# Optimization experiments

Hardware: AMD Instinct MI355X
Metric: run time of the kernel (lower is better)

Reference implementation:

```python
import jax, jax.numpy as jnp
import numpy as np
from jax.scipy.special import erf

F = 64          # scalar feature channels (hidden_irreps multiplicity)
S = 9           # spherical harmonics dim for max_ell=2
NB = 8          # num_bessel
RMAX = 5.0
PPOLY = 5       # num_polynomial_cutoff
AVG_NEIGH = 16.0
SIGMA = 1.0     # atomic_multipoles_smearing_width
KE = 1.0        # Coulomb constant (model units)
N = 20000; G = 20; E = 320000; NEL = 10; L = 2; HMLP = 16

def _sph_l2(u):
    # real spherical harmonics up to l=2, e3nn 'component' normalization,
    # with permute_to_e3nn_convention (y, z, x) ordering for l=1
    x, y, z = u[..., 0], u[..., 1], u[..., 2]
    s3 = 1.7320508075688772; s5 = 2.23606797749979; s15 = 3.872983346207417
    return jnp.stack([jnp.ones_like(x),
                      s3 * y, s3 * z, s3 * x,
                      s15 * x * y, s15 * y * z, 0.5 * s5 * (3.0 * z * z - 1.0),
                      s15 * x * z, 0.5 * s15 * (x * x - y * y)], axis=-1)

def _radial(r):
    # Bessel basis with smooth polynomial cutoff (p = PPOLY)
    n = jnp.arange(1, NB + 1, dtype=r.dtype)
    rb = jnp.sqrt(2.0 / RMAX) * jnp.sin(n * jnp.pi * r[:, None] / RMAX) / r[:, None]
    x = r / RMAX
    p = float(PPOLY)
    u = (1.0 - 0.5 * (p + 1.0) * (p + 2.0) * x**PPOLY
         + p * (p + 2.0) * x**(PPOLY + 1) - 0.5 * p * (p + 1.0) * x**(PPOLY + 2))
    u = jnp.where(x < 1.0, u, 0.0)
    return rb * u[:, None]

def setup_inputs() -> dict:
    key = jax.random.key(0)
    ks = jax.random.split(key, 20)
    Ng = N // G
    species = jax.random.randint(ks[0], (N,), 0, NEL)
    node_attrs = jax.nn.one_hot(species, NEL, dtype=jnp.float32)
    positions = jax.random.uniform(ks[1], (N, 3), dtype=jnp.float32) * 10.0
    g = jax.random.randint(ks[2], (E,), 0, G)
    s_loc = jax.random.randint(ks[3], (E,), 0, Ng)
    off = jax.random.randint(ks[4], (E,), 1, Ng)   # avoid self edges
    r_loc = (s_loc + off) % Ng
    edge_index = jnp.stack([g * Ng + s_loc, g * Ng + r_loc], axis=0)
    batch = jnp.repeat(jnp.arange(G), Ng)
    sc = 0.1
    atomic_energies = jax.random.normal(ks[5], (NEL,)) * sc
    embed_w = jax.random.normal(ks[6], (NEL, F)) * sc
    radial_w1 = jax.random.normal(ks[7], (L, NB, 64)) * 0.3
    radial_b1 = jnp.zeros((L, 64), jnp.float32)
    radial_w2 = jax.random.normal(ks[8], (L, 64, F)) * 0.2
    prod_w = jax.random.normal(ks[9], (L, NEL, F)) * 0.3
    readout_w = jax.random.normal(ks[10], (L, F)) * sc
    ro2_w1 = jax.random.normal(ks[11], (F, HMLP)) * 0.2
    ro2_b1 = jnp.zeros((HMLP,), jnp.float32)
    ro2_w2 = jax.random.normal(ks[12], (HMLP, 1)) * 0.2
    charge_w = jax.random.normal(ks[13], (L, F)) * sc
    flux_w = jax.random.normal(ks[14], (L, NB)) * sc
    formal_charges = jax.random.normal(ks[15], (NEL,)) * 0.5
    return dict(node_attrs=node_attrs, positions=positions, edge_index=edge_index,
                batch=batch, num_graphs=G, atomic_energies=atomic_energies,
                embed_w=embed_w, radial_w1=radial_w1, radial_b1=radial_b1,
                radial_w2=radial_w2, prod_w=prod_w, readout_w=readout_w,
                ro2_w1=ro2_w1, ro2_b1=ro2_b1, ro2_w2=ro2_w2,
                charge_w=charge_w, flux_w=flux_w, formal_charges=formal_charges)

def reference(node_attrs, positions, edge_index, batch, num_graphs,
              atomic_energies, embed_w, radial_w1, radial_b1, radial_w2,
              prod_w, readout_w, ro2_w1, ro2_b1, ro2_w2,
              charge_w, flux_w, formal_charges):
    Nn = node_attrs.shape[0]
    Ng = Nn // num_graphs
    snd, rcv = edge_index[0], edge_index[1]
    # atomic reference energies (E0) and node embedding
    node_e0 = node_attrs @ atomic_energies                      # [N]
    e0 = jax.ops.segment_sum(node_e0, batch, num_graphs)        # [G]
    node_scalars = node_attrs @ embed_w                         # [N,F]
    # edge geometry: gather, spherical harmonics, radial embedding
    vec = positions[rcv] - positions[snd]                       # [E,3]
    lengths = jnp.sqrt((vec * vec).sum(-1) + 1e-12)             # [E]
    unit = vec / lengths[:, None]
    edge_attrs = _sph_l2(unit)                                  # [E,S]
    edge_feats = _radial(lengths)                               # [E,NB]
    # formal charges (per-species)
    FQ = node_attrs @ formal_charges                            # [N]
    charge_density = FQ
    flux = jnp.zeros_like(lengths)
    energies = [e0]
    node_e_list = [node_e0]
    nL = radial_w1.shape[0]
    for l in range(nL):
        # interaction: radial MLP -> per-edge TP messages -> scatter sum
        R = jax.nn.silu(edge_feats @ radial_w1[l] + radial_b1[l]) @ radial_w2[l]  # [E,F]
        m = (R * node_scalars[snd])[:, :, None] * edge_attrs[:, None, :]          # [E,F,S]
        agg = jax.ops.segment_sum(m, rcv, Nn) / AVG_NEIGH                         # [N,F,S]
        # equivariant product (correlation-2 flavor) + element-dependent skip
        sk = node_scalars * (node_attrs @ prod_w[l])                              # [N,F]
        feats = agg + agg * agg[:, :, :1]                                         # [N,F,S]
        node_scalars = feats[:, :, 0] + sk                                        # [N,F]
        if l == nL - 1:
            node_energies = (jax.nn.silu(node_scalars @ ro2_w1 + ro2_b1) @ ro2_w2)[:, 0]
        else:
            node_energies = node_scalars @ readout_w[l]
        energies.append(jax.ops.segment_sum(node_energies, batch, num_graphs))
        node_e_list.append(node_energies)
        # long-range source maps: per-node charge + per-edge flux contributions
        charge_density = charge_density + node_scalars @ charge_w[l]
        flux = flux + edge_feats @ flux_w[l]
    contributions = jnp.stack(energies, -1)                     # [G, L+1]
    total_energy = contributions.sum(-1)                        # [G]
    node_energy = jnp.stack(node_e_list, -1).sum(-1)            # [N]
    # polarization: edge-flux dipole + formal-charge dipole
    pol = jax.ops.segment_sum(flux[:, None] * vec, batch[rcv], num_graphs)
    pol = pol + jax.ops.segment_sum(FQ[:, None] * positions, batch, num_graphs)
    # direct (non-PBC) screened Coulomb energy per graph, equal-size graphs
    q = charge_density.reshape(num_graphs, Ng)
    p = positions.reshape(num_graphs, Ng, 3)
    d = p[:, :, None, :] - p[:, None, :, :]
    r = jnp.sqrt((d * d).sum(-1) + 1e-12)
    kern = erf(r / (2.0 * SIGMA)) / r * (1.0 - jnp.eye(Ng, dtype=r.dtype))
    e_el = 0.5 * KE * jnp.einsum('gi,gij,gj->g', q, kern, q)
    total_energy = total_energy + e_el
    total_charge = jax.ops.segment_sum(charge_density, batch, num_graphs)
    return total_energy, node_energy, contributions, pol, total_charge
```

## Files before the change

kernel.cpp:

```cpp
#include <hip/hip_runtime.h>
#include <math.h>

#define NEL 10
#define FD 64
#define NBES 8
#define GG 20
#define HML 16
#define EGB 512
#define NUB 5000

typedef __attribute__((ext_vector_type(8))) short short8;
typedef __attribute__((ext_vector_type(4))) float f32x4;

__device__ __forceinline__ float wred(float v) {
    #pragma unroll
    for (int off = 32; off > 0; off >>= 1) v += __shfl_down(v, off, 64);
    return v;
}

__device__ __forceinline__ float silu(float h) {
    return h / (1.f + __expf(-h));
}

__device__ __forceinline__ unsigned short f2bf(float x) {
    unsigned int b = __float_as_uint(x);
    unsigned int r = (b + 0x7FFFu + ((b >> 16) & 1u)) >> 16;
    return (unsigned short)r;
}

__device__ __forceinline__ int xcd_swizzle(int bid, int nb) {
    int q = nb >> 3, r = nb & 7;
    int x = bid & 7, i = bid >> 3;
    return (x < r ? x * (q + 1) : r * (q + 1) + (x - r) * q) + i;
}

__global__ __launch_bounds__(256) void setup_k(
    const float* __restrict__ attrs, const float* __restrict__ ae,
    const float* __restrict__ fc, const float* __restrict__ embed_w,
    const int* __restrict__ eidx, int* __restrict__ spec,
    float* __restrict__ q, float* __restrict__ out,
    float* __restrict__ scal, float* __restrict__ agg0,
    int* __restrict__ cnt, int N_, int E_)
{
    int idx = blockIdx.x * 256 + threadIdx.x;
    int lane = threadIdx.x & 63;
    int n = idx >> 6;
    bool pred = (lane < NEL) && (attrs[(size_t)n * NEL + lane] > 0.5f);
    unsigned long long m = __ballot(pred);
    int sp = (int)__builtin_ctzll(m);
    scal[idx] = embed_w[sp * FD + lane];
    agg0[idx] = 0.f;
    if (lane == 0) { spec[n] = sp; q[n] = fc[sp]; out[GG + n] = ae[sp]; }
    if (idx < E_) atomicAdd(&cnt[eidx[E_ + idx]], 1);
    if (idx < GG) out[idx] = 0.f;
}

__global__ __launch_bounds__(1024) void scan_k(
    const int* __restrict__ cnt, int* __restrict__ cur,
    const float* __restrict__ w1, const float* __restrict__ w2,
    unsigned short* __restrict__ w1bf, unsigned short* __restrict__ w2bf, int N_)
{
    int t = threadIdx.x;
    #pragma unroll
    for (int ii = 0; ii < 8; ++ii) {
        int idx = ii * 1024 + t;
        int l = idx >> 12, rem = idx & 4095;
        int f = rem >> 6, k = rem & 63;
        w2bf[idx] = f2bf(w2[l * 4096 + k * 64 + f]);
    }
    {
        int l = t >> 9, rem = t & 511;
        int m = rem >> 3, j = rem & 7;
        w1bf[t] = f2bf(w1[l * 512 + j * 64 + m]);
    }
    __shared__ int wtot[16];
    int lane = t & 63, wid = t >> 6;
    int base = t * 20;
    int c[20]; int s = 0;
    bool full = (base + 20 <= N_);
    if (full) {
        #pragma unroll
        for (int i = 0; i < 5; ++i) {
            int4 v4 = *(const int4*)&cnt[base + i * 4];
            c[i*4+0] = v4.x; c[i*4+1] = v4.y; c[i*4+2] = v4.z; c[i*4+3] = v4.w;
        }
        #pragma unroll
        for (int i = 0; i < 20; ++i) s += c[i];
    } else {
        #pragma unroll
        for (int i = 0; i < 20; ++i) { int idx = base + i; c[i] = (idx < N_) ? cnt[idx] : 0; s += c[i]; }
    }
    int v = s;
    #pragma unroll
    for (int off = 1; off < 64; off <<= 1) {
        int u = __shfl_up(v, off, 64);
        if (lane >= off) v += u;
    }
    if (lane == 63) wtot[wid] = v;
    __syncthreads();
    if (wid == 0 && lane < 16) {
        int wv = wtot[lane];
        #pragma unroll
        for (int off = 1; off < 16; off <<= 1) {
            int u = __shfl_up(wv, off, 64);
            if (lane >= off) wv += u;
        }
        wtot[lane] = wv;
    }
    __syncthreads();
    int ex = (wid > 0 ? wtot[wid - 1] : 0) + (v - s);
    if (full) {
        int o[20];
        #pragma unroll
        for (int i = 0; i < 20; ++i) { o[i] = ex; ex += c[i]; }
        #pragma unroll
        for (int i = 0; i < 5; ++i)
            *(int4*)&cur[base + i * 4] = make_int4(o[i*4+0], o[i*4+1], o[i*4+2], o[i*4+3]);
    } else {
        #pragma unroll
        for (int i = 0; i < 20; ++i) {
            int idx = base + i;
            if (idx < N_) { cur[idx] = ex; ex += c[i]; }
        }
    }
}

__global__ __launch_bounds__(256) void geom_scatter_k(
    const float* __restrict__ pos, const int* __restrict__ eidx,
    const float* __restrict__ flux_w, int* __restrict__ cur,
    unsigned int* __restrict__ esd, float* __restrict__ polpart,
    int E_, int ng)
{
    __shared__ float lpol[GG * 3];
    int tid = threadIdx.x;
    for (int i = tid; i < GG * 3; i += 256) lpol[i] = 0.f;
    __syncthreads();
    float fw[NBES];
    #pragma unroll
    for (int i = 0; i < NBES; ++i) fw[i] = flux_w[i] + flux_w[NBES + i];
    const float PI = 3.14159265358979323846f;
    for (int e = blockIdx.x * 256 + tid; e < E_; e += EGB * 256) {
        int s = eidx[e], r = eidx[E_ + e];
        float dx = pos[(size_t)r*3+0] - pos[(size_t)s*3+0];
        float dy = pos[(size_t)r*3+1] - pos[(size_t)s*3+1];
        float dz = pos[(size_t)r*3+2] - pos[(size_t)s*3+2];
        float len = sqrtf(dx*dx + dy*dy + dz*dz + 1e-12f);
        float x = len * 0.2f;
        float u = 0.f;
        if (x < 1.f) {
            float x2 = x * x;
            float x5 = x2 * x2 * x;
            u = 1.f - 21.f * x5 + 35.f * x5 * x - 15.f * x5 * x2;
        }
        float pref = 0.6324555320336759f / len * u;
        float theta = PI * x;
        float s1, c1;
        __sincosf(theta, &s1, &c1);
        float c2 = 2.f * c1;
        float sp_ = 0.f, sn = s1;
        float flux = 0.f;
        unsigned int pk[4];
        #pragma unroll
        for (int i = 0; i < 4; ++i) {
            float r0 = pref * sn;
            float n1 = c2 * sn - sp_; sp_ = sn; sn = n1;
            float r1 = pref * sn;
            n1 = c2 * sn - sp_; sp_ = sn; sn = n1;
            flux += r0 * fw[2*i] + r1 * fw[2*i+1];
            pk[i] = (unsigned int)f2bf(r0) | ((unsigned int)f2bf(r1) << 16);
        }
        int p = atomicAdd(&cur[r], 1);
        size_t off = (size_t)p * 8;
        *(uint4*)&esd[off]     = make_uint4(pk[0], pk[1], pk[2], pk[3]);
        *(uint2*)&esd[off + 4] = make_uint2((unsigned int)s, (unsigned int)r);
        int g = r / ng;
        atomicAdd(&lpol[g*3+0], flux * dx);
        atomicAdd(&lpol[g*3+1], flux * dy);
        atomicAdd(&lpol[g*3+2], flux * dz);
    }
    __syncthreads();
    for (int i = tid; i < GG * 3; i += 256) polpart[blockIdx.x * (GG * 3) + i] = lpol[i];
}

__global__ __launch_bounds__(256, 6) void edge_mlp_k(
    const unsigned int* __restrict__ esd,
    const unsigned short* __restrict__ w1bf, const float* __restrict__ b1,
    const unsigned short* __restrict__ w2bf, const float* __restrict__ scal,
    float* __restrict__ agg0, int layer, int E_)
{
    __shared__ __align__(16) char smem[4][4352];
    int t = threadIdx.x, w = t >> 6, lane = t & 63;
    int mrow = lane & 15, quad = lane >> 4;
    int xb = xcd_swizzle(blockIdx.x, gridDim.x);
    int ebase = (xb * 4 + w) * 16;
    unsigned short* hw = (unsigned short*)smem[w];
    float* cw = (float*)smem[w];

    int2 sr = *(const int2*)&esd[(size_t)(ebase + mrow) * 8 + 4];
    int sv = sr.x, rv = sr.y;

    const short8 z8 = {0,0,0,0,0,0,0,0};
    short8 b_ef = z8;
    if (quad == 0) b_ef = *(const short8*)&esd[(size_t)(ebase + mrow) * 8];
    else if (quad == 1) b_ef[0] = (short)0x3F80;
    short8 a1f[4];
    #pragma unroll
    for (int nt = 0; nt < 4; ++nt) {
        a1f[nt] = z8;
        if (quad == 0) a1f[nt] = *(const short8*)&w1bf[layer * 512 + (nt * 16 + mrow) * 8];
        else if (quad == 1) a1f[nt][0] = (short)f2bf(b1[layer * FD + nt * 16 + mrow]);
    }

    f32x4 zf = {0.f, 0.f, 0.f, 0.f};
    #pragma unroll
    for (int nt = 0; nt < 4; ++nt) {
        f32x4 c1 = __builtin_amdgcn_mfma_f32_16x16x32_bf16(a1f[nt], b_ef, zf, 0, 0, 0);
        unsigned int p01 = (unsigned int)f2bf(silu(c1[0])) | ((unsigned int)f2bf(silu(c1[1])) << 16);
        unsigned int p23 = (unsigned int)f2bf(silu(c1[2])) | ((unsigned int)f2bf(silu(c1[3])) << 16);
        *(uint2*)&hw[mrow * 72 + nt * 16 + quad * 4] = make_uint2(p01, p23);
    }

    const unsigned short* wb = w2bf + layer * 4096;
    short8 bf0[4], bf1[4];
    #pragma unroll
    for (int nt = 0; nt < 4; ++nt) {
        bf0[nt] = *(const short8*)&wb[(nt * 16 + mrow) * 64 + quad * 8];
        bf1[nt] = *(const short8*)&wb[(nt * 16 + mrow) * 64 + 32 + quad * 8];
    }

    short8 a0  = *(const short8*)&hw[mrow * 72 + quad * 8];
    short8 a1b = *(const short8*)&hw[mrow * 72 + 32 + quad * 8];
    f32x4 c[4];
    #pragma unroll
    for (int nt = 0; nt < 4; ++nt) {
        f32x4 cc = __builtin_amdgcn_mfma_f32_16x16x32_bf16(a0, bf0[nt], zf, 0, 0, 0);
        cc = __builtin_amdgcn_mfma_f32_16x16x32_bf16(a1b, bf1[nt], cc, 0, 0, 0);
        c[nt] = cc;
    }
    #pragma unroll
    for (int nt = 0; nt < 4; ++nt)
        #pragma unroll
        for (int reg = 0; reg < 4; ++reg)
            cw[(quad * 4 + reg) * 68 + nt * 16 + mrow] = c[nt][reg];

    int curR = __builtin_amdgcn_readlane(rv, 0);
    float run = 0.f;
    #pragma unroll
    for (int half = 0; half < 2; ++half) {
        float cv[8], sw[8];
        #pragma unroll
        for (int k = 0; k < 8; ++k) {
            int pp = half * 8 + k;
            cv[k] = cw[pp * 68 + lane];
            int s = __builtin_amdgcn_readlane(sv, pp);
            sw[k] = scal[(size_t)s * FD + lane];
        }
        #pragma unroll
        for (int k = 0; k < 8; ++k) {
            int pp = half * 8 + k;
            int r = __builtin_amdgcn_readlane(rv, pp);
            float v = cv[k] * sw[k];
            if (r != curR) {
                atomicAdd(&agg0[(size_t)curR * FD + lane], run);
                run = v; curR = r;
            } else {
                run += v;
            }
        }
    }
    atomicAdd(&agg0[(size_t)curR * FD + lane], run);
}

__global__ __launch_bounds__(256) void node_update_k(
    float* __restrict__ scal, float* __restrict__ agg0,
    const int* __restrict__ spec, const float* __restrict__ prod_w,
    const float* __restrict__ readout_w, const float* __restrict__ ro2_w1,
    const float* __restrict__ ro2_b1, const float* __restrict__ ro2_w2,
    const float* __restrict__ charge_w, float* __restrict__ q,
    float* __restrict__ out_nodeE, float* __restrict__ nEpart,
    int layer, int last, int N_)
{
    __shared__ float vsh[4][FD];
    __shared__ float red[4];
    int wid = threadIdx.x >> 6, lane = threadIdx.x & 63;
    int n = blockIdx.x * 4 + wid;
    int sp = spec[n];
    size_t idx = (size_t)n * FD + lane;
    float a = agg0[idx] * 0.0625f;
    if (!last) agg0[idx] = 0.f;
    float v = a + a * a + scal[idx] * prod_w[(layer * NEL + sp) * FD + lane];
    scal[idx] = v;

    float ne;
    if (!last) {
        ne = wred(v * readout_w[layer * FD + lane]);
    } else {
        vsh[wid][lane] = v;
        float h = 0.f;
        if (lane < HML) {
            h = ro2_b1[lane];
            for (int ff = 0; ff < FD; ++ff) h += vsh[wid][ff] * ro2_w1[ff * HML + lane];
            h = silu(h) * ro2_w2[lane];
        }
        ne = wred(h);
    }
    float qs = wred(v * charge_w[layer * FD + lane]);
    if (lane == 0) {
        out_nodeE[n] += ne;
        q[n] += qs;
        red[wid] = ne;
    }
    __syncthreads();
    if (threadIdx.x == 0) nEpart[layer * NUB + blockIdx.x] = red[0] + red[1] + red[2] + red[3];
}

__global__ __launch_bounds__(256) void coulomb_final_k(
    const float* __restrict__ q, const float* __restrict__ pos,
    const int* __restrict__ spec, const float* __restrict__ ae,
    const float* __restrict__ fc, const float* __restrict__ nEpart,
    const float* __restrict__ polpart, float* __restrict__ out,
    int N_, int ng)
{
    __shared__ float sh[260];
    int vb = blockIdx.x;
    int g = vb / 137, rem = vb % 137;
    int t = threadIdx.x, lane = t & 63, w = t >> 6;

    if (rem < 136) {
        int a = 0, r2 = rem;
        while (r2 >= 16 - a) { r2 -= 16 - a; ++a; }
        int b = a + r2;
        const float* qg = q + (size_t)g * ng;
        const float* pg = pos + (size_t)g * ng * 3;
        float* qs_ = sh; float* jx = sh + 64; float* jy = sh + 128; float* jz = sh + 192;
        if (t < 64) {
            int j = b * 64 + t;
            bool ok = j < ng;
            qs_[t] = ok ? qg[j] : 0.f;
            jx[t] = ok ? pg[(size_t)j*3+0] : 0.f;
            jy[t] = ok ? pg[(size_t)j*3+1] : 0.f;
            jz[t] = ok ? pg[(size_t)j*3+2] : 0.f;
        }
        __syncthreads();
        int i = a * 64 + lane;
        float accu = 0.f;
        if (i < ng) {
            float qi = qg[i];
            float xi = pg[(size_t)i*3+0], yi = pg[(size_t)i*3+1], zi = pg[(size_t)i*3+2];
            #pragma unroll 4
            for (int k = 0; k < 16; ++k) {
                int jj = w * 16 + k;
                int j = b * 64 + jj;
                float dx = xi - jx[jj], dy = yi - jy[jj], dz = zi - jz[jj];
                float d2 = dx*dx + dy*dy + dz*dz + 1e-12f;
                float rinv = __frsqrt_rn(d2);
                float r = d2 * rinv;
                float x = 0.5f * r;
                float tt = __frcp_rn(1.f + 0.3275911f * x);
                float poly = ((((1.061405429f*tt - 1.453152027f)*tt + 1.421413741f)*tt
                               - 0.284496736f)*tt + 0.254829592f)*tt;
                float erfv = 1.f - poly * __expf(-x * x);
                float kern = (j == i) ? 0.f : erfv * rinv;
                accu += qi * qs_[jj] * kern;
            }
        }
        accu = wred(accu);
        if (lane == 0) sh[256 + w] = accu;
        __syncthreads();
        if (t == 0) {
            float s = sh[256] + sh[257] + sh[258] + sh[259];
            atomicAdd(&out[g], (a == b) ? 0.5f * s : s);
        }
    } else {
        float se0 = 0.f, sq = 0.f, p0 = 0.f, p1 = 0.f, p2 = 0.f, s0 = 0.f, s1 = 0.f;
        for (int n = g * ng + t; n < (g + 1) * ng; n += 256) {
            int sp = spec[n];
            float fq = fc[sp];
            se0 += ae[sp];
            sq += q[n];
            p0 += fq * pos[(size_t)n*3+0];
            p1 += fq * pos[(size_t)n*3+1];
            p2 += fq * pos[(size_t)n*3+2];
        }
        if (t < 250) {
            int b = g * 250 + t;
            s0 = nEpart[b];
            s1 = nEpart[NUB + b];
        }
        for (int b = t; b < EGB; b += 256) {
            p0 += polpart[b * (GG * 3) + g * 3 + 0];
            p1 += polpart[b * (GG * 3) + g * 3 + 1];
            p2 += polpart[b * (GG * 3) + g * 3 + 2];
        }
        float vals[7] = {se0, s0, s1, sq, p0, p1, p2};
        float* red = sh;
        #pragma unroll
        for (int k = 0; k < 7; ++k) {
            float r = wred(vals[k]);
            if (lane == 0) red[w * 8 + k] = r;
        }
        __syncthreads();
        if (t < 7) sh[64 + t] = red[t] + red[8 + t] + red[16 + t] + red[24 + t];
        __syncthreads();
        if (t == 0) {
            float a0 = sh[64], a1 = sh[65], a2 = sh[66];
            atomicAdd(&out[g], a0 + a1 + a2);
            float* contrib = out + GG + N_;
            contrib[g*3+0] = a0; contrib[g*3+1] = a1; contrib[g*3+2] = a2;
            float* pol = contrib + GG * 3;
            pol[g*3+0] = sh[68]; pol[g*3+1] = sh[69]; pol[g*3+2] = sh[70];
            float* qt = pol + GG * 3;
            qt[g] = sh[67];
        }
    }
}

extern "C" void kernel_launch(void* const* d_in, const int* in_sizes, int n_in,
                              void* d_out, int out_size, void* d_ws, size_t ws_size,
                              hipStream_t stream)
{
    const float* node_attrs      = (const float*)d_in[0];
    const float* positions       = (const float*)d_in[1];
    const int*   edge_index      = (const int*)d_in[2];
    const float* atomic_energies = (const float*)d_in[5];
    const float* embed_w         = (const float*)d_in[6];
    const float* radial_w1       = (const float*)d_in[7];
    const float* radial_b1       = (const float*)d_in[8];
    const float* radial_w2       = (const float*)d_in[9];
    const float* prod_w          = (const float*)d_in[10];
    const float* readout_w       = (const float*)d_in[11];
    const float* ro2_w1          = (const float*)d_in[12];
    const float* ro2_b1          = (const float*)d_in[13];
    const float* ro2_w2          = (const float*)d_in[14];
    const float* charge_w        = (const float*)d_in[15];
    const float* flux_w          = (const float*)d_in[16];
    const float* formal_charges  = (const float*)d_in[17];

    int N = in_sizes[0] / NEL;
    int E = in_sizes[2] / 2;
    int ng = N / GG;

    float* ws      = (float*)d_ws;
    float* scal    = ws;
    float* agg0    = scal + (size_t)N * FD;
    unsigned int* esd = (unsigned int*)(agg0 + (size_t)N * FD);
    float* q       = (float*)(esd + (size_t)E * 8);
    int*   spec    = (int*)(q + N);
    float* nEpart  = (float*)(spec + N);
    float* polpart = nEpart + 2 * NUB;
    int*   cnt     = (int*)(polpart + EGB * (GG * 3));
    int*   cur     = cnt + N;
    unsigned short* w2bf = (unsigned short*)(cur + N);
    unsigned short* w1bf = w2bf + 8192;

    float* out = (float*)d_out;
    float* out_nodeE = out + GG;

    hipMemsetAsync(cnt, 0, (size_t)N * sizeof(int), stream);

    setup_k<<<(N * FD) / 256, 256, 0, stream>>>(
        node_attrs, atomic_energies, formal_charges, embed_w, edge_index,
        spec, q, out, scal, agg0, cnt, N, E);
    scan_k<<<1, 1024, 0, stream>>>(cnt, cur, radial_w1, radial_w2, w1bf, w2bf, N);
    geom_scatter_k<<<EGB, 256, 0, stream>>>(
        positions, edge_index, flux_w, cur, esd, polpart, E, ng);

    for (int l = 0; l < 2; ++l) {
        edge_mlp_k<<<E / 64, 256, 0, stream>>>(
            esd, w1bf, radial_b1, w2bf, scal, agg0, l, E);
        node_update_k<<<N / 4, 256, 0, stream>>>(
            scal, agg0, spec, prod_w, readout_w, ro2_w1, ro2_b1, ro2_w2,
            charge_w, q, out_nodeE, nEpart, l, (l == 1) ? 1 : 0, N);
    }

    coulomb_final_k<<<GG * 137, 256, 0, stream>>>(
        q, positions, spec, atomic_energies, formal_charges,
        nEpart, polpart, out, N, ng);
}
```

Baseline: 271.3 us.

## Process four edge tiles per wave in edge MLP and move weight conversion into setup

Each wave in the edge MLP kernel now loops over four 16-edge groups instead of one. This amortizes the per-wave weight-fragment loads (w1, b1, w2) and carries the running receiver sum across groups, so fewer partial atomics are flushed at group boundaries. The grid shrinks to a quarter and the occupancy hint is lowered from 6 to 4. The bf16 weight conversion moves from the single-block scan kernel into the wide setup kernel, which shortens the serial scan. The cost is less parallelism per launch and a sequential dependency inside each wave.

```diff
diff --git a/kernel.cpp b/kernel.cpp
--- a/kernel.cpp
+++ b/kernel.cpp
@@ -40,7 +40,10 @@
     const int* __restrict__ eidx, int* __restrict__ spec,
     float* __restrict__ q, float* __restrict__ out,
     float* __restrict__ scal, float* __restrict__ agg0,
-    int* __restrict__ cnt, int N_, int E_)
+    int* __restrict__ cnt,
+    const float* __restrict__ w1, const float* __restrict__ w2,
+    unsigned short* __restrict__ w1bf, unsigned short* __restrict__ w2bf,
+    int N_, int E_)
 {
     int idx = blockIdx.x * 256 + threadIdx.x;
     int lane = threadIdx.x & 63;
@@ -53,26 +56,22 @@
     if (lane == 0) { spec[n] = sp; q[n] = fc[sp]; out[GG + n] = ae[sp]; }
     if (idx < E_) atomicAdd(&cnt[eidx[E_ + idx]], 1);
     if (idx < GG) out[idx] = 0.f;
-}
-
-__global__ __launch_bounds__(1024) void scan_k(
-    const int* __restrict__ cnt, int* __restrict__ cur,
-    const float* __restrict__ w1, const float* __restrict__ w2,
-    unsigned short* __restrict__ w1bf, unsigned short* __restrict__ w2bf, int N_)
-{
-    int t = threadIdx.x;
-    #pragma unroll
-    for (int ii = 0; ii < 8; ++ii) {
-        int idx = ii * 1024 + t;
+    if (idx < 8192) {
         int l = idx >> 12, rem = idx & 4095;
         int f = rem >> 6, k = rem & 63;
         w2bf[idx] = f2bf(w2[l * 4096 + k * 64 + f]);
-    }
-    {
-        int l = t >> 9, rem = t & 511;
-        int m = rem >> 3, j = rem & 7;
-        w1bf[t] = f2bf(w1[l * 512 + j * 64 + m]);
-    }
+    } else if (idx < 9216) {
+        int j = idx - 8192;
+        int l = j >> 9, rem = j & 511;
+        int mm = rem >> 3, jj = rem & 7;
+        w1bf[j] = f2bf(w1[l * 512 + jj * 64 + mm]);
+    }
+}
+
+__global__ __launch_bounds__(1024) void scan_k(
+    const int* __restrict__ cnt, int* __restrict__ cur, int N_)
+{
+    int t = threadIdx.x;
     __shared__ int wtot[16];
     int lane = t & 63, wid = t >> 6;
     int base = t * 20;
@@ -182,7 +181,7 @@
     for (int i = tid; i < GG * 3; i += 256) polpart[blockIdx.x * (GG * 3) + i] = lpol[i];
 }
 
-__global__ __launch_bounds__(256, 6) void edge_mlp_k(
+__global__ __launch_bounds__(256, 4) void edge_mlp_k(
     const unsigned int* __restrict__ esd,
     const unsigned short* __restrict__ w1bf, const float* __restrict__ b1,
     const unsigned short* __restrict__ w2bf, const float* __restrict__ scal,
@@ -192,17 +191,11 @@
     int t = threadIdx.x, w = t >> 6, lane = t & 63;
     int mrow = lane & 15, quad = lane >> 4;
     int xb = xcd_swizzle(blockIdx.x, gridDim.x);
-    int ebase = (xb * 4 + w) * 16;
+    int wbase = (xb * 4 + w) * 64;
     unsigned short* hw = (unsigned short*)smem[w];
     float* cw = (float*)smem[w];
 
-    int2 sr = *(const int2*)&esd[(size_t)(ebase + mrow) * 8 + 4];
-    int sv = sr.x, rv = sr.y;
-
     const short8 z8 = {0,0,0,0,0,0,0,0};
-    short8 b_ef = z8;
-    if (quad == 0) b_ef = *(const short8*)&esd[(size_t)(ebase + mrow) * 8];
-    else if (quad == 1) b_ef[0] = (short)0x3F80;
     short8 a1f[4];
     #pragma unroll
     for (int nt = 0; nt < 4; ++nt) {
@@ -210,16 +203,6 @@
         if (quad == 0) a1f[nt] = *(const short8*)&w1bf[layer * 512 + (nt * 16 + mrow) * 8];
         else if (quad == 1) a1f[nt][0] = (short)f2bf(b1[layer * FD + nt * 16 + mrow]);
     }
-
-    f32x4 zf = {0.f, 0.f, 0.f, 0.f};
-    #pragma unroll
-    for (int nt = 0; nt < 4; ++nt) {
-        f32x4 c1 = __builtin_amdgcn_mfma_f32_16x16x32_bf16(a1f[nt], b_ef, zf, 0, 0, 0);
-        unsigned int p01 = (unsigned int)f2bf(silu(c1[0])) | ((unsigned int)f2bf(silu(c1[1])) << 16);
-        unsigned int p23 = (unsigned int)f2bf(silu(c1[2])) | ((unsigned int)f2bf(silu(c1[3])) << 16);
-        *(uint2*)&hw[mrow * 72 + nt * 16 + quad * 4] = make_uint2(p01, p23);
-    }
-
     const unsigned short* wb = w2bf + layer * 4096;
     short8 bf0[4], bf1[4];
     #pragma unroll
@@ -228,43 +211,65 @@
         bf1[nt] = *(const short8*)&wb[(nt * 16 + mrow) * 64 + 32 + quad * 8];
     }
 
-    short8 a0  = *(const short8*)&hw[mrow * 72 + quad * 8];
-    short8 a1b = *(const short8*)&hw[mrow * 72 + 32 + quad * 8];
-    f32x4 c[4];
-    #pragma unroll
-    for (int nt = 0; nt < 4; ++nt) {
-        f32x4 cc = __builtin_amdgcn_mfma_f32_16x16x32_bf16(a0, bf0[nt], zf, 0, 0, 0);
-        cc = __builtin_amdgcn_mfma_f32_16x16x32_bf16(a1b, bf1[nt], cc, 0, 0, 0);
-        c[nt] = cc;
-    }
-    #pragma unroll
-    for (int nt = 0; nt < 4; ++nt)
-        #pragma unroll
-        for (int reg = 0; reg < 4; ++reg)
-            cw[(quad * 4 + reg) * 68 + nt * 16 + mrow] = c[nt][reg];
-
-    int curR = __builtin_amdgcn_readlane(rv, 0);
+    f32x4 zf = {0.f, 0.f, 0.f, 0.f};
+    int curR = -1;
     float run = 0.f;
-    #pragma unroll
-    for (int half = 0; half < 2; ++half) {
-        float cv[8], sw[8];
-        #pragma unroll
-        for (int k = 0; k < 8; ++k) {
-            int pp = half * 8 + k;
-            cv[k] = cw[pp * 68 + lane];
-            int s = __builtin_amdgcn_readlane(sv, pp);
-            sw[k] = scal[(size_t)s * FD + lane];
-        }
-        #pragma unroll
-        for (int k = 0; k < 8; ++k) {
-            int pp = half * 8 + k;
-            int r = __builtin_amdgcn_readlane(rv, pp);
-            float v = cv[k] * sw[k];
-            if (r != curR) {
-                atomicAdd(&agg0[(size_t)curR * FD + lane], run);
-                run = v; curR = r;
-            } else {
-                run += v;
+
+    #pragma unroll 1
+    for (int grp = 0; grp < 4; ++grp) {
+        int ebase = wbase + grp * 16;
+        int2 sr = *(const int2*)&esd[(size_t)(ebase + mrow) * 8 + 4];
+        int sv = sr.x, rv = sr.y;
+        if (grp == 0) curR = __builtin_amdgcn_readlane(rv, 0);
+
+        short8 b_ef = z8;
+        if (quad == 0) b_ef = *(const short8*)&esd[(size_t)(ebase + mrow) * 8];
+        else if (quad == 1) b_ef[0] = (short)0x3F80;
+
+        #pragma unroll
+        for (int nt = 0; nt < 4; ++nt) {
+            f32x4 c1 = __builtin_amdgcn_mfma_f32_16x16x32_bf16(a1f[nt], b_ef, zf, 0, 0, 0);
+            unsigned int p01 = (unsigned int)f2bf(silu(c1[0])) | ((unsigned int)f2bf(silu(c1[1])) << 16);
+            unsigned int p23 = (unsigned int)f2bf(silu(c1[2])) | ((unsigned int)f2bf(silu(c1[3])) << 16);
+            *(uint2*)&hw[mrow * 72 + nt * 16 + quad * 4] = make_uint2(p01, p23);
+        }
+
+        short8 a0  = *(const short8*)&hw[mrow * 72 + quad * 8];
+        short8 a1b = *(const short8*)&hw[mrow * 72 + 32 + quad * 8];
+        f32x4 c[4];
+        #pragma unroll
+        for (int nt = 0; nt < 4; ++nt) {
+            f32x4 cc = __builtin_amdgcn_mfma_f32_16x16x32_bf16(a0, bf0[nt], zf, 0, 0, 0);
+            cc = __builtin_amdgcn_mfma_f32_16x16x32_bf16(a1b, bf1[nt], cc, 0, 0, 0);
+            c[nt] = cc;
+        }
+        #pragma unroll
+        for (int nt = 0; nt < 4; ++nt)
+            #pragma unroll
+            for (int reg = 0; reg < 4; ++reg)
+                cw[(quad * 4 + reg) * 68 + nt * 16 + mrow] = c[nt][reg];
+
+        #pragma unroll
+        for (int half = 0; half < 2; ++half) {
+            float cv[8], sw[8];
+            #pragma unroll
+            for (int k = 0; k < 8; ++k) {
+                int pp = half * 8 + k;
+                cv[k] = cw[pp * 68 + lane];
+                int s = __builtin_amdgcn_readlane(sv, pp);
+                sw[k] = scal[(size_t)s * FD + lane];
+            }
+            #pragma unroll
+            for (int k = 0; k < 8; ++k) {
+                int pp = half * 8 + k;
+                int r = __builtin_amdgcn_readlane(rv, pp);
+                float v = cv[k] * sw[k];
+                if (r != curR) {
+                    atomicAdd(&agg0[(size_t)curR * FD + lane], run);
+                    run = v; curR = r;
+                } else {
+                    run += v;
+                }
             }
         }
     }
@@ -460,13 +465,13 @@
 
     setup_k<<<(N * FD) / 256, 256, 0, stream>>>(
         node_attrs, atomic_energies, formal_charges, embed_w, edge_index,
-        spec, q, out, scal, agg0, cnt, N, E);
-    scan_k<<<1, 1024, 0, stream>>>(cnt, cur, radial_w1, radial_w2, w1bf, w2bf, N);
+        spec, q, out, scal, agg0, cnt, radial_w1, radial_w2, w1bf, w2bf, N, E);
+    scan_k<<<1, 1024, 0, stream>>>(cnt, cur, N);
     geom_scatter_k<<<EGB, 256, 0, stream>>>(
         positions, edge_index, flux_w, cur, esd, polpart, E, ng);
 
     for (int l = 0; l < 2; ++l) {
-        edge_mlp_k<<<E / 64, 256, 0, stream>>>(
+        edge_mlp_k<<<E / 256, 256, 0, stream>>>(
             esd, w1bf, radial_b1, w2bf, scal, agg0, l, E);
         node_update_k<<<N / 4, 256, 0, stream>>>(
             scal, agg0, spec, prod_w, readout_w, ro2_w1, ro2_b1, ro2_w2,
```

After: 263.5 us. 1.03x faster.
